# Kernel optimization log

Hardware: AMD Instinct MI355X
Metric: run time of the kernel (lower is better)

The kernel has to match this reference:

```python
import jax, jax.numpy as jnp
import numpy as np

L, B, T, D, V = 4, 32, 512, 512, 1000


def setup_inputs() -> dict:
    key = jax.random.key(0)
    k0, k1, k2, k3, k4 = jax.random.split(key, 5)
    ids = jax.random.randint(k0, (B, T), 0, V)
    mask = jax.random.randint(k1, (B, T), 0, 2).astype(bool)  # True = valid token
    emb = jax.random.normal(k2, (V, D), dtype=jnp.float32) * 0.1
    W = jax.random.normal(k3, (L, D, 3 * D), dtype=jnp.float32) / np.float32(np.sqrt(D))
    v = jax.random.normal(k4, (L, 2, D), dtype=jnp.float32) * 0.1  # (v_f, v_r) per layer
    b = jnp.zeros((L, 2, D), dtype=jnp.float32)                    # (b_f, b_r) per layer
    return {"ids": ids, "mask": mask, "emb": emb, "W": W, "v": v, "b": b}


def _sru_layer(x, pad, Wl, vf, vr, bf, br):
    # x: [T,B,D] layer input; pad: [T,B,1] bool (True = padded step)
    Tn, Bn, Dn = x.shape
    U = jnp.einsum('tbd,de->tbe', x, Wl).reshape(Tn, Bn, 3, Dn)
    xt, fpre, rpre = U[:, :, 0], U[:, :, 1], U[:, :, 2]

    def step(c, inp):
        xt_t, fp_t, rp_t, x_t, pad_t = inp
        f = jax.nn.sigmoid(fp_t + vf * c + bf)
        r = jax.nn.sigmoid(rp_t + vr * c + br)
        c_new = f * c + (1.0 - f) * xt_t
        h = r * jnp.tanh(c_new) + (1.0 - r) * x_t  # highway (input_size==hidden_size)
        c_out = jnp.where(pad_t, c, c_new)          # padded step: keep state
        h = jnp.where(pad_t, 0.0, h)                # padded step: zero output
        return c_out, h

    c0 = jnp.zeros_like(x[0])  # zero initial hidden state, as in the torch code
    _, h = jax.lax.scan(step, c0, (xt, fpre, rpre, x, pad))
    return h  # [T,B,D]


def reference(ids, mask, emb, W, v, b):
    x = emb[ids]                       # CharEmbedder lookup: [B,T,D]
    x = jnp.transpose(x, (1, 0, 2))    # [T,B,D]  (permute(1,0,2))
    pad = (~mask).T[:, :, None]        # inverted_mask.T -> [T,B,1]
    for l in range(L):
        x = _sru_layer(x, pad, W[l], v[l, 0], v[l, 1], b[l, 0], b[l, 1])
    return jnp.transpose(x, (1, 0, 2))  # back to [B,T,D]
```

## Files before the change

### kernel.cpp

```cpp
#include <hip/hip_runtime.h>
#include <hip/hip_bf16.h>


#define LAYERS 4
#define BB 32
#define TT 512
#define DD 512
#define N3 1536
#define MROWS (TT * BB)
#define WPL ((size_t)DD * N3)
#define SB 32
#define LOG2E 1.4426950408889634f
#define TWOLOG2E 2.8853900817779268f

typedef unsigned short u16;
typedef unsigned int u32;
typedef _Float16 half8 __attribute__((ext_vector_type(8)));
typedef float f32x4 __attribute__((ext_vector_type(4)));

#define SBAR() asm volatile("s_barrier" ::: "memory")
#define WAITVM(n) asm volatile("s_waitcnt vmcnt(" n ")" ::: "memory")

__device__ __forceinline__ float b2f(u16 u) {
  union { unsigned int i; float f; } x;
  x.i = ((unsigned int)u) << 16;
  return x.f;
}
__device__ __forceinline__ u16 f2h(float f) {
  _Float16 h = (_Float16)f;
  return *(u16*)&h;
}
__device__ __forceinline__ float h2f(u16 u) {
  _Float16 h;
  *(u16*)&h = u;
  return (float)h;
}
__device__ __forceinline__ float rcpf(float x) { return __builtin_amdgcn_rcpf(x); }
__device__ __forceinline__ float exp2f_(float x) { return __builtin_amdgcn_exp2f(x); }

__device__ __forceinline__ void async_ld16(const void* g, void* l) {
  __builtin_amdgcn_global_load_lds(
      (const __attribute__((address_space(1))) void*)g,
      (__attribute__((address_space(3))) void*)l, 16, 0, 0);
}
__device__ __forceinline__ void async_ld4(const void* g, void* l) {
  __builtin_amdgcn_global_load_lds(
      (const __attribute__((address_space(1))) void*)g,
      (__attribute__((address_space(3))) void*)l, 4, 0, 0);
}

__global__ void detect_kernel(const u16* __restrict__ emb_u,
                              const int* __restrict__ mask_i,
                              const int* __restrict__ ids_i,
                              int* __restrict__ flags) {
  __shared__ int cnt[3];
  __shared__ int zc;
  int tid = threadIdx.x;
  if (tid < 3) cnt[tid] = 0;
  if (tid == 0) zc = 0;
  __syncthreads();
  int bad = 0, zero_even = 0;
  for (int i = tid; i < 8192; i += 256) {
    u16 u = emb_u[i];
    unsigned e = (u >> 7) & 0xFF;
    if (e >= 0x8F) bad++;
    if ((i & 1) == 0 && u == 0) zero_even++;
  }
  if (bad) atomicAdd(&cnt[0], bad);
  if (zero_even) atomicAdd(&zc, zero_even);
  if (tid < 64) {
    unsigned vv = (unsigned)mask_i[tid];
    if (vv > 1u) atomicAdd(&cnt[1], 1);
  }
  if (tid < 256) {
    if (ids_i[2 * tid + 1] == 0) atomicAdd(&cnt[2], 1);
  }
  __syncthreads();
  if (tid == 0) {
    flags[0] = (cnt[0] > 64 || zc > 3000) ? 1 : 0;
    flags[1] = (cnt[1] > 0) ? 1 : 0;
    flags[2] = (cnt[2] >= 192) ? 1 : 0;
  }
}

__global__ __launch_bounds__(256)
void wprep_kernel(const void* __restrict__ W, u16* __restrict__ W16,
                  const int* __restrict__ flags) {
  __shared__ float tileW[32][33];
  int l = blockIdx.z;
  int k0 = blockIdx.x * 32;
  int n0 = blockIdx.y * 32;
  int tx = threadIdx.x & 31;
  int ty = threadIdx.x >> 5;
  int ff = flags[0];
  const float* Wf = (const float*)W + (size_t)l * WPL;
  const u16* Wb = (const u16*)W + (size_t)l * WPL;
  for (int kk = ty; kk < 32; kk += 8) {
    size_t off = (size_t)(k0 + kk) * N3 + n0 + tx;
    tileW[kk][tx] = ff ? Wf[off] : b2f(Wb[off]);
  }
  __syncthreads();
  u16* outP = W16 + (size_t)l * WPL;
  for (int nn = ty; nn < 32; nn += 8) {
    float x = tileW[tx][nn];
    outP[(size_t)(n0 + nn) * DD + k0 + tx] = f2h(x);
  }
}

__global__ void embed_kernel(const int* __restrict__ ids,
                             const void* __restrict__ emb,
                             u16* __restrict__ X16,
                             const int* __restrict__ flags) {
  int i = blockIdx.x * 256 + threadIdx.x;
  int d = i & (DD - 1);
  int tb = i >> 9;
  int b = tb & (BB - 1);
  int t = tb >> 5;
  int ii = b * TT + t;
  int id = flags[2] ? ids[2 * ii] : ids[ii];
  float val = flags[0] ? ((const float*)emb)[id * DD + d]
                       : b2f(((const u16*)emb)[id * DD + d]);
  X16[i] = f2h(val);
}

__global__ __launch_bounds__(256, 2)
void gemm_kernel(const u16* __restrict__ X16, const u16* __restrict__ W16l,
                 const void* __restrict__ bvec, int layer,
                 const int* __restrict__ flags,
                 u16* __restrict__ U16, int row_base, int chunkM, int nblk) {
  __shared__ u16 ldsA[3][8192];
  __shared__ u16 ldsB[3][4096];
  const int tid = threadIdx.x;
  const int lane = tid & 63, wave = tid >> 6;
  const int wm = wave >> 1, wn = wave & 1;
  const int m16 = lane & 15, quad = lane >> 4;

  const int orig = blockIdx.x;
  const int wg = (orig & 7) * (nblk >> 3) + (orig >> 3);
  const int mt = wg / 12, nt = wg - mt * 12;

  const int arow0 = row_base + mt * 256;
  const int bcol0 = nt * 128;

  const int srow = lane >> 2;
  const int sq = (lane & 3) ^ ((lane >> 3) & 3);
  const u16* pa = X16 + (size_t)(arow0 + wave * 64 + srow) * DD + sq * 8;
  const u16* pb = W16l + (size_t)(bcol0 + wave * 32 + srow) * DD + sq * 8;

  auto stage = [&](int t) {
    const int sl = t % 3;
    const int kv = t * 32;
    u16* da = &ldsA[sl][(wave * 4) * 512];
    const u16* sa = pa + kv;
#pragma unroll
    for (int j = 0; j < 4; ++j)
      async_ld16(sa + (size_t)16 * j * DD, da + j * 512);
    u16* db_ = &ldsB[sl][(wave * 2) * 512];
    const u16* sb = pb + kv;
#pragma unroll
    for (int j = 0; j < 2; ++j)
      async_ld16(sb + (size_t)16 * j * DD, db_ + j * 512);
  };

  f32x4 acc[8][4];
#pragma unroll
  for (int mi = 0; mi < 8; ++mi)
#pragma unroll
    for (int ni = 0; ni < 4; ++ni)
#pragma unroll
      for (int r = 0; r < 4; ++r) acc[mi][ni][r] = 0.f;

  stage(0); stage(1);
  WAITVM("6");
  SBAR();

  const int loff = m16 * 32 + (quad ^ ((m16 >> 1) & 3)) * 8;

#pragma unroll
  for (int t = 0; t < 16; ++t) {
    const int sl = t % 3;
    half8 af[8], bf[4];
#pragma unroll
    for (int i = 0; i < 8; ++i)
      af[i] = *(const half8*)&ldsA[sl][(wm * 8 + i) * 512 + loff];
#pragma unroll
    for (int i = 0; i < 4; ++i)
      bf[i] = *(const half8*)&ldsB[sl][(wn * 4 + i) * 512 + loff];
    if (t + 2 < 16) stage(t + 2);
    __builtin_amdgcn_s_setprio(1);
#pragma unroll
    for (int mi = 0; mi < 8; ++mi)
#pragma unroll
      for (int ni = 0; ni < 4; ++ni)
        acc[mi][ni] = __builtin_amdgcn_mfma_f32_16x16x32_f16(
            af[mi], bf[ni], acc[mi][ni], 0, 0, 0);
    __builtin_amdgcn_s_setprio(0);
    if (t <= 13) WAITVM("6");
    else if (t == 14) WAITVM("0");
    if (t < 15) SBAR();
  }

  const int ff = flags[0];
  const int pl = nt >> 2;
  const int dd0 = (nt & 3) * 128;
  u16* up = U16 + (size_t)pl * chunkM * 512;
  const int r0 = mt * 256 + wm * 128 + quad * 4;
  const int c0 = dd0 + wn * 64 + m16;
  if (pl == 0) {
#pragma unroll
    for (int mi = 0; mi < 8; ++mi)
#pragma unroll
      for (int reg = 0; reg < 4; ++reg) {
        size_t rb = (size_t)(r0 + mi * 16 + reg) * 512 + c0;
#pragma unroll
        for (int ni = 0; ni < 4; ++ni)
          up[rb + ni * 16] = f2h(acc[mi][ni][reg]);
      }
  } else {
    float bias[4];
#pragma unroll
    for (int ni = 0; ni < 4; ++ni) {
      size_t bo = (size_t)layer * 2 * DD + (size_t)(pl - 1) * DD + c0 + ni * 16;
      bias[ni] = ff ? ((const float*)bvec)[bo] : b2f(((const u16*)bvec)[bo]);
    }
#pragma unroll
    for (int mi = 0; mi < 8; ++mi)
#pragma unroll
      for (int reg = 0; reg < 4; ++reg) {
        size_t rb = (size_t)(r0 + mi * 16 + reg) * 512 + c0;
#pragma unroll
        for (int ni = 0; ni < 4; ++ni)
          up[rb + ni * 16] = f2h(-(acc[mi][ni][reg] + bias[ni]) * LOG2E);
      }
  }
}

template <int EMIT>
__global__ __launch_bounds__(448, 1)
void scan_kernel(const u16* __restrict__ U16, float* __restrict__ X,
                 u16* __restrict__ X16,
                 const void* __restrict__ mask_p, const void* __restrict__ vbase,
                 int layer, const int* __restrict__ flags,
                 float* __restrict__ carry, int t0, int nt, int chunkM) {
  __shared__ u16 bufA[2][2][SB][64];
  __shared__ u16 bufB[3][2][SB][64];
  __shared__ float ring[2][2][SB][64];
  __shared__ int msk[TT];
  const int tid = threadIdx.x;
  const int wave = tid >> 6, lane = tid & 63;
  const int idx0 = blockIdx.x * 64;
  const int b = idx0 >> 9;
  const int d0 = idx0 & 511;
  const int ff = flags[0], fm = flags[1];

  const int* mi_ = (const int*)mask_p + b * TT;
  const unsigned char* mb_ = (const unsigned char*)mask_p + b * TT;
  for (int i = tid; i < nt; i += 448) msk[i] = fm ? (int)mb_[t0 + i] : mi_[t0 + i];

  float vfs = 0.f, vrs = 0.f, c = 0.f;
  {
    int d = d0 + lane;
    size_t voff = (size_t)layer * 2 * DD;
    if (wave == 0) {
      float vf = ff ? ((const float*)vbase)[voff + d]
                    : b2f(((const u16*)vbase)[voff + d]);
      vfs = -vf * LOG2E;
      c = (t0 == 0) ? 0.f : carry[idx0 + lane];
    } else if (wave >= 1 && wave <= 4) {
      float vr = ff ? ((const float*)vbase)[voff + DD + d]
                    : b2f(((const u16*)vbase)[voff + DD + d]);
      vrs = -vr * LOG2E;
    }
  }

  const int nbuf = nt / SB;

  auto ld_pair = [&](const u16* rowS, const u16* rowS1, void* ldst) {
    const u32* a0 = (const u32*)rowS;
    const u32* a1 = (const u32*)rowS1;
    const u32* ga = (lane < 32) ? (a0 + lane) : (a1 + (lane - 32));
    async_ld4(ga, ldst);
  };

  auto produceA = [&](int k) {
    int ph = k & 1, tl = k * SB;
    const u16* p0 = U16 + ((size_t)tl * BB + b) * 512 + d0;
    const u16* p1 = p0 + (size_t)chunkM * 512;
#pragma unroll
    for (int s = 0; s < SB; s += 2)
      ld_pair(p0 + (size_t)s * BB * 512, p0 + (size_t)(s + 1) * BB * 512,
              &bufA[ph][0][s][0]);
#pragma unroll
    for (int s = 0; s < SB; s += 2)
      ld_pair(p1 + (size_t)s * BB * 512, p1 + (size_t)(s + 1) * BB * 512,
              &bufA[ph][1][s][0]);
  };
  auto produceB = [&](int k) {
    int ph = k % 3, tl = k * SB;
    const u16* p2 = U16 + 2 * (size_t)chunkM * 512 + ((size_t)tl * BB + b) * 512 + d0;
    const u16* xb = X16 + ((size_t)(t0 + tl) * BB + b) * DD + d0;
#pragma unroll
    for (int s = 0; s < SB; s += 2)
      ld_pair(p2 + (size_t)s * BB * 512, p2 + (size_t)(s + 1) * BB * 512,
              &bufB[ph][0][s][0]);
#pragma unroll
    for (int s = 0; s < SB; s += 2)
      ld_pair(xb + (size_t)s * BB * DD, xb + (size_t)(s + 1) * BB * DD,
              &bufB[ph][1][s][0]);
  };

  float* Xp = X + (size_t)b * TT * DD + d0 + lane;

  auto hphase = [&](int j, int hw) {
    int phc = j & 1, phb = j % 3;
    int sbase = hw * (SB / 4);
#pragma unroll
    for (int si = 0; si < SB / 4; ++si) {
      int s = sbase + si;
      float cprev = ring[phc][0][s][lane];
      float cn = ring[phc][1][s][lane];
      float rps = h2f(bufB[phb][0][s][lane]);
      float xin = h2f(bufB[phb][1][s][lane]);
      int m = msk[j * SB + s];
      float tr = exp2f_(fmaf(vrs, cprev, rps));
      float r = rcpf(1.f + tr);
      float e2 = exp2f_(cn * TWOLOG2E);
      float th = fmaf(-2.f, rcpf(e2 + 1.f), 1.f);
      float h = fmaf(r, th - xin, xin);
      float hout = (m == 0) ? 0.f : h;
      int tg = t0 + j * SB + s;
      if (EMIT)
        X16[((size_t)tg * BB + b) * DD + d0 + lane] = f2h(hout);
      else
        Xp[(size_t)tg * DD] = hout;
    }
  };

  if (wave == 5) produceA(0);
  if (wave == 6) produceB(0);

  for (int k = 0; k < nbuf; ++k) {
    __syncthreads();
    if (wave == 5) {
      if (k + 1 < nbuf) produceA(k + 1);
    } else if (wave == 6) {
      if (k + 1 < nbuf) produceB(k + 1);
    } else if (wave == 0) {
      int ph = k & 1;
#pragma unroll 8
      for (int s = 0; s < SB; ++s) {
        float xt = h2f(bufA[ph][0][s][lane]);
        float fps = h2f(bufA[ph][1][s][lane]);
        float t = exp2f_(fmaf(vfs, c, fps));
        float f = rcpf(1.f + t);
        float cn = fmaf(f, c - xt, xt);
        ring[ph][0][s][lane] = c;
        ring[ph][1][s][lane] = cn;
        c = (msk[k * SB + s] == 0) ? c : cn;
      }
    } else {
      if (k > 0) hphase(k - 1, wave - 1);
    }
  }
  __syncthreads();
  if (wave >= 1 && wave <= 4) hphase(nbuf - 1, wave - 1);
  if (wave == 0) carry[idx0 + lane] = c;
}

__global__ void sentinel_kernel(float* out) { out[threadIdx.x] = 12345.f; }

extern "C" void kernel_launch(void* const* d_in, const int* in_sizes, int n_in,
                              void* d_out, int out_size, void* d_ws, size_t ws_size,
                              hipStream_t stream) {
  const int* ids = (const int*)d_in[0];
  const void* mask = d_in[1];
  const void* emb = d_in[2];
  const void* W = d_in[3];
  const void* v = d_in[4];
  const void* bp = d_in[5];

  char* ws = (char*)d_ws;
  int* flags = (int*)ws;
  float* carry = (float*)(ws + 4096);
  const size_t offX16 = 69632;
  const size_t offW16 = offX16 + (size_t)MROWS * DD * 2;
  const size_t offU = offW16 + (size_t)LAYERS * WPL * 2;
  const size_t perT = (size_t)BB * N3 * 2;

  const int cand[4] = {512, 256, 128, 64};
  int chunkT = 0;
  for (int i = 0; i < 4; ++i) {
    if (ws_size >= offU + (size_t)cand[i] * perT) { chunkT = cand[i]; break; }
  }
  if (!chunkT) {
    sentinel_kernel<<<1, 256, 0, stream>>>((float*)d_out);
    return;
  }
  const int chunkM = chunkT * BB;

  u16* X16 = (u16*)(ws + offX16);
  u16* W16 = (u16*)(ws + offW16);
  u16* U16 = (u16*)(ws + offU);
  float* X = (float*)d_out;

  detect_kernel<<<1, 256, 0, stream>>>((const u16*)emb, (const int*)mask,
                                       (const int*)ids, flags);
  wprep_kernel<<<dim3(16, 48, 4), 256, 0, stream>>>(W, W16, flags);
  embed_kernel<<<MROWS * DD / 256, 256, 0, stream>>>(ids, emb, X16, flags);

  int nch = TT / chunkT;
  for (int l = 0; l < LAYERS; ++l) {
    const u16* W16l = W16 + (size_t)l * WPL;
    for (int ch = 0; ch < nch; ++ch) {
      int t0 = ch * chunkT;
      int nblk = (chunkM / 256) * 12;
      gemm_kernel<<<nblk, 256, 0, stream>>>(X16, W16l, bp, l, flags, U16,
                                            t0 * BB, chunkM, nblk);
      if (l < LAYERS - 1)
        scan_kernel<1><<<BB * DD / 64, 448, 0, stream>>>(U16, X, X16, mask, v, l,
                                                         flags, carry, t0, chunkT,
                                                         chunkM);
      else
        scan_kernel<0><<<BB * DD / 64, 448, 0, stream>>>(U16, X, X16, mask, v, l,
                                                         flags, carry, t0, chunkT,
                                                         chunkM);
    }
  }
}
```

Baseline: 348.4 us.

## Fold h-phase into single recurrence wave and shrink scan block to three waves

The scan kernel drops the separate h-computation waves and the LDS ring buffer. One wave now computes both the c recurrence and the h output per step, while two producer waves prefetch 64-step double-buffered tiles and synchronise with raw s_barrier plus vmcnt waits. The aim is to cut per-block LDS traffic, barrier count and thread count so more blocks fit per CU. The cost is that the r/tanh/h math and global stores now sit on the serial critical path of the recurrence wave.

```diff
diff --git a/kernel.cpp b/kernel.cpp
--- a/kernel.cpp
+++ b/kernel.cpp
@@ -9,7 +9,7 @@
 #define N3 1536
 #define MROWS (TT * BB)
 #define WPL ((size_t)DD * N3)
-#define SB 32
+#define SB2 64
 #define LOG2E 1.4426950408889634f
 #define TWOLOG2E 2.8853900817779268f
 
@@ -236,15 +236,14 @@
 }
 
 template <int EMIT>
-__global__ __launch_bounds__(448, 1)
+__global__ __launch_bounds__(192, 1)
 void scan_kernel(const u16* __restrict__ U16, float* __restrict__ X,
                  u16* __restrict__ X16,
                  const void* __restrict__ mask_p, const void* __restrict__ vbase,
                  int layer, const int* __restrict__ flags,
                  float* __restrict__ carry, int t0, int nt, int chunkM) {
-  __shared__ u16 bufA[2][2][SB][64];
-  __shared__ u16 bufB[3][2][SB][64];
-  __shared__ float ring[2][2][SB][64];
+  __shared__ u16 bufA[2][2][SB2][64];
+  __shared__ u16 bufB[2][2][SB2][64];
   __shared__ int msk[TT];
   const int tid = threadIdx.x;
   const int wave = tid >> 6, lane = tid & 63;
@@ -255,25 +254,22 @@
 
   const int* mi_ = (const int*)mask_p + b * TT;
   const unsigned char* mb_ = (const unsigned char*)mask_p + b * TT;
-  for (int i = tid; i < nt; i += 448) msk[i] = fm ? (int)mb_[t0 + i] : mi_[t0 + i];
+  for (int i = tid; i < nt; i += 192) msk[i] = fm ? (int)mb_[t0 + i] : mi_[t0 + i];
 
   float vfs = 0.f, vrs = 0.f, c = 0.f;
-  {
+  if (wave == 0) {
     int d = d0 + lane;
     size_t voff = (size_t)layer * 2 * DD;
-    if (wave == 0) {
-      float vf = ff ? ((const float*)vbase)[voff + d]
-                    : b2f(((const u16*)vbase)[voff + d]);
-      vfs = -vf * LOG2E;
-      c = (t0 == 0) ? 0.f : carry[idx0 + lane];
-    } else if (wave >= 1 && wave <= 4) {
-      float vr = ff ? ((const float*)vbase)[voff + DD + d]
-                    : b2f(((const u16*)vbase)[voff + DD + d]);
-      vrs = -vr * LOG2E;
-    }
-  }
-
-  const int nbuf = nt / SB;
+    float vf = ff ? ((const float*)vbase)[voff + d]
+                  : b2f(((const u16*)vbase)[voff + d]);
+    float vr = ff ? ((const float*)vbase)[voff + DD + d]
+                  : b2f(((const u16*)vbase)[voff + DD + d]);
+    vfs = -vf * LOG2E;
+    vrs = -vr * LOG2E;
+    c = (t0 == 0) ? 0.f : carry[idx0 + lane];
+  }
+
+  const int nbuf = nt / SB2;
 
   auto ld_pair = [&](const u16* rowS, const u16* rowS1, void* ldst) {
     const u32* a0 = (const u32*)rowS;
@@ -283,87 +279,76 @@
   };
 
   auto produceA = [&](int k) {
-    int ph = k & 1, tl = k * SB;
+    int ph = k & 1, tl = k * SB2;
     const u16* p0 = U16 + ((size_t)tl * BB + b) * 512 + d0;
     const u16* p1 = p0 + (size_t)chunkM * 512;
 #pragma unroll
-    for (int s = 0; s < SB; s += 2)
+    for (int s = 0; s < SB2; s += 2)
       ld_pair(p0 + (size_t)s * BB * 512, p0 + (size_t)(s + 1) * BB * 512,
               &bufA[ph][0][s][0]);
 #pragma unroll
-    for (int s = 0; s < SB; s += 2)
+    for (int s = 0; s < SB2; s += 2)
       ld_pair(p1 + (size_t)s * BB * 512, p1 + (size_t)(s + 1) * BB * 512,
               &bufA[ph][1][s][0]);
   };
   auto produceB = [&](int k) {
-    int ph = k % 3, tl = k * SB;
+    int ph = k & 1, tl = k * SB2;
     const u16* p2 = U16 + 2 * (size_t)chunkM * 512 + ((size_t)tl * BB + b) * 512 + d0;
     const u16* xb = X16 + ((size_t)(t0 + tl) * BB + b) * DD + d0;
 #pragma unroll
-    for (int s = 0; s < SB; s += 2)
+    for (int s = 0; s < SB2; s += 2)
       ld_pair(p2 + (size_t)s * BB * 512, p2 + (size_t)(s + 1) * BB * 512,
               &bufB[ph][0][s][0]);
 #pragma unroll
-    for (int s = 0; s < SB; s += 2)
+    for (int s = 0; s < SB2; s += 2)
       ld_pair(xb + (size_t)s * BB * DD, xb + (size_t)(s + 1) * BB * DD,
               &bufB[ph][1][s][0]);
   };
 
-  float* Xp = X + (size_t)b * TT * DD + d0 + lane;
-
-  auto hphase = [&](int j, int hw) {
-    int phc = j & 1, phb = j % 3;
-    int sbase = hw * (SB / 4);
-#pragma unroll
-    for (int si = 0; si < SB / 4; ++si) {
-      int s = sbase + si;
-      float cprev = ring[phc][0][s][lane];
-      float cn = ring[phc][1][s][lane];
-      float rps = h2f(bufB[phb][0][s][lane]);
-      float xin = h2f(bufB[phb][1][s][lane]);
-      int m = msk[j * SB + s];
-      float tr = exp2f_(fmaf(vrs, cprev, rps));
-      float r = rcpf(1.f + tr);
-      float e2 = exp2f_(cn * TWOLOG2E);
-      float th = fmaf(-2.f, rcpf(e2 + 1.f), 1.f);
-      float h = fmaf(r, th - xin, xin);
-      float hout = (m == 0) ? 0.f : h;
-      int tg = t0 + j * SB + s;
-      if (EMIT)
-        X16[((size_t)tg * BB + b) * DD + d0 + lane] = f2h(hout);
-      else
-        Xp[(size_t)tg * DD] = hout;
+  const size_t SU = (size_t)BB * 512;
+  u16* pxw = X16 + ((size_t)t0 * BB + b) * DD + d0 + lane;
+  float* pX = X + ((size_t)b * TT + t0) * DD + d0 + lane;
+
+  if (wave == 1) produceA(0);
+  if (wave == 2) produceB(0);
+  __syncthreads();
+
+  for (int k = 0; k < nbuf; ++k) {
+    if (wave == 1) {
+      if (k + 1 < nbuf) produceA(k + 1);
+      WAITVM("0");
+      SBAR();
+    } else if (wave == 2) {
+      if (k + 1 < nbuf) produceB(k + 1);
+      WAITVM("0");
+      SBAR();
+    } else {
+      const int ph = k & 1;
+      const int tb0 = k * SB2;
+#pragma unroll 8
+      for (int s = 0; s < SB2; ++s) {
+        const float xt = h2f(bufA[ph][0][s][lane]);
+        const float fps = h2f(bufA[ph][1][s][lane]);
+        const float rps = h2f(bufB[ph][0][s][lane]);
+        const float xi = h2f(bufB[ph][1][s][lane]);
+        const int m = msk[tb0 + s];
+        const float tf = exp2f_(fmaf(vfs, c, fps));
+        const float f = rcpf(1.f + tf);
+        const float cn = fmaf(f, c - xt, xt);
+        const float tr = exp2f_(fmaf(vrs, c, rps));
+        const float r = rcpf(1.f + tr);
+        const float e2 = exp2f_(cn * TWOLOG2E);
+        const float th = fmaf(-2.f, rcpf(e2 + 1.f), 1.f);
+        const float h = fmaf(r, th - xi, xi);
+        const float hout = (m == 0) ? 0.f : h;
+        const int tg = tb0 + s;
+        if (EMIT) pxw[(size_t)tg * SU] = f2h(hout);
+        else pX[(size_t)tg * DD] = hout;
+        c = (m == 0) ? c : cn;
+      }
+      SBAR();
     }
-  };
-
-  if (wave == 5) produceA(0);
-  if (wave == 6) produceB(0);
-
-  for (int k = 0; k < nbuf; ++k) {
-    __syncthreads();
-    if (wave == 5) {
-      if (k + 1 < nbuf) produceA(k + 1);
-    } else if (wave == 6) {
-      if (k + 1 < nbuf) produceB(k + 1);
-    } else if (wave == 0) {
-      int ph = k & 1;
-#pragma unroll 8
-      for (int s = 0; s < SB; ++s) {
-        float xt = h2f(bufA[ph][0][s][lane]);
-        float fps = h2f(bufA[ph][1][s][lane]);
-        float t = exp2f_(fmaf(vfs, c, fps));
-        float f = rcpf(1.f + t);
-        float cn = fmaf(f, c - xt, xt);
-        ring[ph][0][s][lane] = c;
-        ring[ph][1][s][lane] = cn;
-        c = (msk[k * SB + s] == 0) ? c : cn;
-      }
-    } else {
-      if (k > 0) hphase(k - 1, wave - 1);
-    }
-  }
-  __syncthreads();
-  if (wave >= 1 && wave <= 4) hphase(nbuf - 1, wave - 1);
+  }
   if (wave == 0) carry[idx0 + lane] = c;
 }
 
@@ -417,11 +402,11 @@
       gemm_kernel<<<nblk, 256, 0, stream>>>(X16, W16l, bp, l, flags, U16,
                                             t0 * BB, chunkM, nblk);
       if (l < LAYERS - 1)
-        scan_kernel<1><<<BB * DD / 64, 448, 0, stream>>>(U16, X, X16, mask, v, l,
+        scan_kernel<1><<<BB * DD / 64, 192, 0, stream>>>(U16, X, X16, mask, v, l,
                                                          flags, carry, t0, chunkT,
                                                          chunkM);
       else
-        scan_kernel<0><<<BB * DD / 64, 448, 0, stream>>>(U16, X, X16, mask, v, l,
+        scan_kernel<0><<<BB * DD / 64, 192, 0, stream>>>(U16, X, X16, mask, v, l,
                                                          flags, carry, t0, chunkT,
                                                          chunkM);
     }
```

After: 413.7 us. 18.7% more time.
